# Performance work log

Measured on AMD Instinct MI355X. Metric: run time of the kernel, lower is better.

Reference implementation:

```python
import jax, jax.numpy as jnp
import numpy as np

PHI = (1.0 + 5.0 ** 0.5) / 2.0
B, S, V, D, N, L = 8, 128, 32000, 256, 256, 2


def silu(x):
    return x * jax.nn.sigmoid(x)


def setup_inputs() -> dict:
    key = jax.random.key(0)
    ks = jax.random.split(key, 9)
    inp = {}
    inp["input_ids"] = jax.random.randint(ks[0], (B, S), 0, V)
    # token embedding, init std=0.02 as in _init_weights
    inp["emb"] = 0.02 * jax.random.normal(ks[1], (V, 2 * D), jnp.float32)
    # per-layer resonant params, stacked over layer dim L
    inp["ip_w"] = 0.02 * jax.random.normal(ks[2], (L, D, 2 * D), jnp.float32)  # input_proj weight
    inp["ip_b"] = jnp.zeros((L, D), jnp.float32)                                # input_proj bias
    inp["Wn"] = 0.02 * jax.random.normal(ks[3], (L, N, D), jnp.float32)         # W parameter
    inp["Bn"] = jnp.zeros((L, N, D), jnp.float32)                               # B parameter
    inp["opr"] = 0.02 * jax.random.normal(ks[4], (L, D, N), jnp.float32)        # out_proj_real
    inp["opi"] = 0.02 * jax.random.normal(ks[5], (L, D, N), jnp.float32)        # out_proj_imag
    inp["out_w"] = 0.02 * jax.random.normal(ks[6], (V, 2 * D), jnp.float32)     # output_proj
    inp["out_b"] = jnp.zeros((V,), jnp.float32)
    return inp


def _forward(input_ids, emb, ip_w, ip_b, Wn, Bn, opr, opi, out_w, out_b):
    tok = emb[input_ids]                                  # [B, S, 2D]
    w_emb = jnp.transpose(tok[..., :D], (1, 0, 2))        # [S, B, D] (time-major for scan)
    b_emb = jnp.transpose(tok[..., D:], (1, 0, 2))        # [S, B, D]
    ts = jnp.arange(S, dtype=jnp.float32)                 # t values

    def step(carry, xs):
        h_r, h_i = carry
        w_t, b_t, t = xs
        t_phi = t * PHI
        # Euler transform of recurrent state
        wl = 1.0 + jnp.abs(w_t)                           # [B, D]
        th_r = h_r / wl + b_t + t_phi
        th_i = h_i / wl + b_t + t_phi
        sr, cr = jnp.sin(th_r), jnp.cos(th_r)
        si, ci = jnp.sin(th_i), jnp.cos(th_i)
        h_r_new = cr * ci - sr * si                       # complex rotate
        h_i_new = cr * si + sr * ci
        x_r, x_i = h_r_new, h_i_new
        # resonant layers (residual deltas)
        for l in range(L):
            xc = jnp.concatenate([x_r, x_i], axis=-1) @ ip_w[l].T + ip_b[l]   # [B, D]
            wl_n = 1.0 + jnp.abs(Wn[l])                                        # [N, D]
            theta = xc[:, None, :] / wl_n + Bn[l] + t_phi                      # [B, N, D]
            cos_sum = jnp.cos(theta).sum(-1)                                   # [B, N]
            sin_sum = jnp.sin(theta).sum(-1)                                   # [B, N]
            x_r = x_r + silu(cos_sum @ opr[l].T)
            x_i = x_i + silu(sin_sum @ opi[l].T)
        logits = jnp.concatenate([x_r, x_i], axis=-1) @ out_w.T + out_b       # [B, V]
        return (h_r_new, h_i_new), logits

    h0 = jnp.zeros((B, D), jnp.float32)
    (_, _), logits = jax.lax.scan(step, (h0, h0), (w_emb, b_emb, ts))
    return jnp.transpose(logits, (1, 0, 2))               # [B, S, V]


def reference(input_ids, emb, ip_w, ip_b, Wn, Bn, opr, opi, out_w, out_b):
    return _forward(input_ids, emb, ip_w, ip_b, Wn, Bn, opr, opi, out_w, out_b)
```

## Files before the change

### kernel.cpp

```cpp
#include <hip/hip_runtime.h>
#include <hip/hip_fp16.h>
#include <math.h>


#define PHIF 1.6180339887498949f

typedef unsigned short u16;
typedef __attribute__((ext_vector_type(8))) _Float16 f16x8;
typedef __attribute__((ext_vector_type(4))) float f32x4;

constexpr int B = 8, S = 128, V = 32000, D = 256, N = 256, L = 2;
constexpr int TWO_D = 512;
constexpr int M = S * B;

constexpr size_t OFF_XR   = 0;
constexpr size_t OFF_XI   = OFF_XR   + (size_t)M * D;
constexpr size_t OFF_XC   = OFF_XI   + (size_t)M * D;
constexpr size_t OFF_CS   = OFF_XC   + (size_t)M * D;
constexpr size_t OFF_SS   = OFF_CS   + (size_t)M * N;
constexpr size_t OFF_RWT  = OFF_SS   + (size_t)M * N;
constexpr size_t OFF_BNT  = OFF_RWT  + (size_t)L * N * D;
constexpr size_t OFF_IPWT = OFF_BNT  + (size_t)L * N * D;
constexpr size_t OFF_OPRT = OFF_IPWT + (size_t)L * TWO_D * D;
constexpr size_t OFF_OPIT = OFF_OPRT + (size_t)L * N * D;
constexpr size_t OFF_FLT_END = OFF_OPIT + (size_t)L * N * D;

constexpr size_t A2_BYTE_OFF = OFF_FLT_END * 4;
constexpr size_t W2_BYTE_OFF = A2_BYTE_OFF + (size_t)M * 512 * 2;
constexpr size_t WS_NEED     = W2_BYTE_OFF + (size_t)V * 512 * 2;

__device__ __forceinline__ u16 f2h(float x) {
    return __half_as_ushort(__float2half(x));
}

__global__ __launch_bounds__(256) void prepconv_kernel(const float* __restrict__ Wn,
                                                       const float* __restrict__ Bn,
                                                       const float* __restrict__ ip_w,
                                                       const float* __restrict__ opr,
                                                       const float* __restrict__ opi,
                                                       const float* __restrict__ out_w,
                                                       float* __restrict__ ws,
                                                       u16* __restrict__ W2) {
    int blk = blockIdx.x;
    if (blk < 1024) {
        int i = blk * 256 + threadIdx.x;
        if (i < L * N * D) {
            int l = i >> 16;
            int r = i & 65535;
            int a = r >> 8;
            int c = r & 255;
            float wv = Wn[(size_t)l * N * D + (size_t)c * D + a];
            ws[OFF_RWT + i] = 1.0f / (1.0f + fabsf(wv));
            ws[OFF_BNT + i] = Bn[(size_t)l * N * D + (size_t)c * D + a];
            ws[OFF_OPRT + i] = opr[(size_t)l * D * N + (size_t)c * N + a];
            ws[OFF_OPIT + i] = opi[(size_t)l * D * N + (size_t)c * N + a];
        }
        int l = i >> 17;
        int r = i & 131071;
        int k = r >> 8;
        int d = r & 255;
        ws[OFF_IPWT + i] = ip_w[(size_t)l * D * TWO_D + (size_t)d * TWO_D + k];
    } else {
        int gid = (blk - 1024) * 256 + threadIdx.x;
        if (gid >= V * 128) return;
        int v  = gid >> 7;
        int kq = (gid & 127) << 2;
        float4 x = *(const float4*)&out_w[(size_t)v * TWO_D + kq];
        ushort4 h = {f2h(x.x), f2h(x.y), f2h(x.z), f2h(x.w)};
        *(ushort4*)&W2[(size_t)v * 512 + kq] = h;
    }
}

__global__ __launch_bounds__(64) void recur_kernel(const int* __restrict__ ids,
                                                   const float* __restrict__ emb,
                                                   float* __restrict__ ws) {
    __shared__ int   sid[S];
    __shared__ float swv[S][64];
    __shared__ float sbv[S][64];
    int lane = threadIdx.x;
    int blk  = blockIdx.x;
    int b  = blk >> 2;
    int d  = (blk & 3) * 64 + lane;
    sid[lane]      = ids[b * S + lane];
    sid[64 + lane] = ids[b * S + 64 + lane];
    __syncthreads();
    #pragma unroll 16
    for (int t = 0; t < S; ++t) {
        const float* e = emb + (size_t)sid[t] * TWO_D;
        swv[t][lane] = e[d];
        sbv[t][lane] = e[D + d];
    }
    __syncthreads();
    float* XR = ws + OFF_XR;
    float* XI = ws + OFF_XI;
    float u = 0.f;
    #pragma unroll 8
    for (int t = 0; t < S; ++t) {
        float wl = 1.0f + fabsf(swv[t][lane]);
        float c  = 2.0f * sbv[t][lane] + (2.0f * PHIF) * (float)t;
        float psi = __fdividef(u, wl) + c;
        float sn = __sinf(psi);
        float cs = __cosf(psi);
        size_t row = (size_t)(t * B + b) * D + d;
        XR[row] = cs;
        XI[row] = sn;
        u = cs + sn;
    }
}

__global__ __launch_bounds__(256) void layers_kernel(const float* __restrict__ ipb,
                                                     float* __restrict__ ws,
                                                     u16* __restrict__ A2,
                                                     int use_a2) {
    __shared__ float xr[4][D];
    __shared__ float xi[4][D];
    __shared__ float xc[4][D];
    __shared__ float cs[4][N];
    __shared__ float ss[4][N];
    int m0 = blockIdx.x * 4;
    int tid = threadIdx.x;

    #pragma unroll
    for (int r = 0; r < 4; ++r) {
        xr[r][tid] = ws[OFF_XR + (size_t)(m0 + r) * D + tid];
        xi[r][tid] = ws[OFF_XI + (size_t)(m0 + r) * D + tid];
    }
    float tp[4];
    #pragma unroll
    for (int r = 0; r < 4; ++r) tp[r] = (float)((m0 + r) >> 3) * PHIF;

    for (int l = 0; l < L; ++l) {
        __syncthreads();
        const float* WT = ws + OFF_IPWT + (size_t)l * TWO_D * D;
        float bias = ipb[l * D + tid];
        float a[4];
        #pragma unroll
        for (int r = 0; r < 4; ++r) a[r] = bias;
        #pragma unroll 4
        for (int k = 0; k < D; ++k) {
            float wv = WT[k * D + tid];
            #pragma unroll
            for (int r = 0; r < 4; ++r) a[r] = fmaf(xr[r][k], wv, a[r]);
        }
        #pragma unroll 4
        for (int k = 0; k < D; ++k) {
            float wv = WT[(k + D) * D + tid];
            #pragma unroll
            for (int r = 0; r < 4; ++r) a[r] = fmaf(xi[r][k], wv, a[r]);
        }
        #pragma unroll
        for (int r = 0; r < 4; ++r) xc[r][tid] = a[r];
        __syncthreads();

        const float* RW = ws + OFF_RWT + (size_t)l * D * N;
        const float* BN = ws + OFF_BNT + (size_t)l * D * N;
        float ac[4] = {0.f, 0.f, 0.f, 0.f};
        float as[4] = {0.f, 0.f, 0.f, 0.f};
        #pragma unroll 2
        for (int d = 0; d < D; ++d) {
            float rw = RW[d * N + tid];
            float bn = BN[d * N + tid];
            #pragma unroll
            for (int r = 0; r < 4; ++r) {
                float th = fmaf(xc[r][d], rw, bn) + tp[r];
                ac[r] += __cosf(th);
                as[r] += __sinf(th);
            }
        }
        #pragma unroll
        for (int r = 0; r < 4; ++r) { cs[r][tid] = ac[r]; ss[r][tid] = as[r]; }
        __syncthreads();

        const float* WR = ws + OFF_OPRT + (size_t)l * N * D;
        const float* WI = ws + OFF_OPIT + (size_t)l * N * D;
        float ur[4] = {0.f, 0.f, 0.f, 0.f};
        float ui[4] = {0.f, 0.f, 0.f, 0.f};
        #pragma unroll 4
        for (int n = 0; n < N; ++n) {
            float wr = WR[n * D + tid];
            float wi = WI[n * D + tid];
            #pragma unroll
            for (int r = 0; r < 4; ++r) {
                ur[r] = fmaf(cs[r][n], wr, ur[r]);
                ui[r] = fmaf(ss[r][n], wi, ui[r]);
            }
        }
        #pragma unroll
        for (int r = 0; r < 4; ++r) {
            float vr = ur[r], vi = ui[r];
            float sgr = 1.0f / (1.0f + expf(-vr));
            float sgi = 1.0f / (1.0f + expf(-vi));
            xr[r][tid] += vr * sgr;
            xi[r][tid] += vi * sgi;
        }
    }
    __syncthreads();
    #pragma unroll
    for (int r = 0; r < 4; ++r) {
        ws[OFF_XR + (size_t)(m0 + r) * D + tid] = xr[r][tid];
        ws[OFF_XI + (size_t)(m0 + r) * D + tid] = xi[r][tid];
    }
    if (use_a2) {
        #pragma unroll
        for (int r = 0; r < 4; ++r) {
            A2[(size_t)(m0 + r) * 512 + tid]       = f2h(xr[r][tid]);
            A2[(size_t)(m0 + r) * 512 + 256 + tid] = f2h(xi[r][tid]);
        }
    }
}

__global__ __launch_bounds__(256) void logits_mfma_kernel(const u16* __restrict__ A2,
                                                          const u16* __restrict__ W2,
                                                          const float* __restrict__ out_b,
                                                          float* __restrict__ out) {
    __shared__ u16 sA[128 * 32];
    __shared__ u16 sW[128 * 32];
    int rb = blockIdx.x & 7;
    int cb = blockIdx.x >> 3;
    int tid = threadIdx.x;
    int w = tid >> 6, l = tid & 63;
    int wr = w >> 1, wc = w & 1;

    f32x4 acc[4][4];
    #pragma unroll
    for (int i = 0; i < 4; ++i)
        #pragma unroll
        for (int j = 0; j < 4; ++j) acc[i][j] = (f32x4){0.f, 0.f, 0.f, 0.f};

    int srow = l >> 2;
    int sko  = (l & 3) * 8;
    int kg = (l >> 4) * 8;
    int rl = l & 15;

    for (int kk = 0; kk < 512; kk += 32) {
        #pragma unroll
        for (int j = 0; j < 2; ++j) {
            int rloc = (w * 2 + j) * 16 + srow;
            const u16* sa = A2 + (size_t)(rb * 128 + rloc) * 512 + kk + sko;
            const u16* sw = W2 + (size_t)(cb * 128 + rloc) * 512 + kk + sko;
            u16* da = &sA[rloc * 32 + sko];
            u16* dw = &sW[rloc * 32 + sko];
            __builtin_amdgcn_global_load_lds((const __attribute__((address_space(1))) void*)sa,
                                             (__attribute__((address_space(3))) void*)da, 16, 0, 0);
            __builtin_amdgcn_global_load_lds((const __attribute__((address_space(1))) void*)sw,
                                             (__attribute__((address_space(3))) void*)dw, 16, 0, 0);
        }
        __syncthreads();
        f16x8 af[4], wf[4];
        #pragma unroll
        for (int f = 0; f < 4; ++f) {
            af[f] = *(const f16x8*)&sA[(wr * 64 + f * 16 + rl) * 32 + kg];
            wf[f] = *(const f16x8*)&sW[(wc * 64 + f * 16 + rl) * 32 + kg];
        }
        #pragma unroll
        for (int fr = 0; fr < 4; ++fr)
            #pragma unroll
            for (int fc = 0; fc < 4; ++fc)
                acc[fr][fc] = __builtin_amdgcn_mfma_f32_16x16x32_f16(
                    af[fr], wf[fc], acc[fr][fc], 0, 0, 0);
        __syncthreads();
    }

    int rq = l >> 4;
    #pragma unroll
    for (int fc = 0; fc < 4; ++fc) {
        int v = cb * 128 + wc * 64 + fc * 16 + rl;
        float bv = out_b[v];
        #pragma unroll
        for (int fr = 0; fr < 4; ++fr) {
            #pragma unroll
            for (int r = 0; r < 4; ++r) {
                int row = rb * 128 + wr * 64 + fr * 16 + rq * 4 + r;
                int t = row >> 3, b = row & 7;
                out[((size_t)(b * S + t)) * V + v] = acc[fr][fc][r] + bv;
            }
        }
    }
}

constexpr int GBM = 256, GBN = 64, GBK = 32;
constexpr int LDA = GBM + 4;
constexpr int LDW = GBN + 4;

__global__ __launch_bounds__(256) void logits_kernel(const float* __restrict__ out_w,
                                                     const float* __restrict__ out_b,
                                                     const float* __restrict__ ws,
                                                     float* __restrict__ out) {
    __shared__ float As[GBK][LDA];
    __shared__ float Wsh[GBK][LDW];
    const float* XR = ws + OFF_XR;
    const float* XI = ws + OFF_XI;
    int cb = blockIdx.x % (V / GBN);
    int rb = blockIdx.x / (V / GBN);
    int tid = threadIdx.x;
    int tx = tid & 7;
    int ty = tid >> 3;
    int m_base = ty * 8;
    int n0 = tx * 8;
    float acc[8][8];
    #pragma unroll
    for (int r = 0; r < 8; ++r)
        #pragma unroll
        for (int c = 0; c < 8; ++c) acc[r][c] = 0.f;

    for (int kc = 0; kc < TWO_D; kc += GBK) {
        #pragma unroll
        for (int j = 0; j < 32; ++j) {
            int idx = tid + j * 256;
            int k = idx & 31;
            int m = idx >> 5;
            int kgl = kc + k;
            int row = rb * GBM + m;
            As[k][m] = (kgl < D) ? XR[row * D + kgl] : XI[row * D + (kgl - D)];
        }
        #pragma unroll
        for (int j = 0; j < 8; ++j) {
            int idx = tid + j * 256;
            int k = idx & 31;
            int n = idx >> 5;
            Wsh[k][n] = out_w[(size_t)(cb * GBN + n) * TWO_D + kc + k];
        }
        __syncthreads();
        #pragma unroll 8
        for (int k = 0; k < GBK; ++k) {
            float4 a0 = *(const float4*)&As[k][m_base];
            float4 a1 = *(const float4*)&As[k][m_base + 4];
            float4 w0 = *(const float4*)&Wsh[k][n0];
            float4 w1 = *(const float4*)&Wsh[k][n0 + 4];
            float am[8] = {a0.x, a0.y, a0.z, a0.w, a1.x, a1.y, a1.z, a1.w};
            float wn[8] = {w0.x, w0.y, w0.z, w0.w, w1.x, w1.y, w1.z, w1.w};
            #pragma unroll
            for (int r = 0; r < 8; ++r)
                #pragma unroll
                for (int c = 0; c < 8; ++c)
                    acc[r][c] = fmaf(am[r], wn[c], acc[r][c]);
        }
        __syncthreads();
    }
    int v0 = cb * GBN + n0;
    float4 ob0 = *(const float4*)&out_b[v0];
    float4 ob1 = *(const float4*)&out_b[v0 + 4];
    float obn[8] = {ob0.x, ob0.y, ob0.z, ob0.w, ob1.x, ob1.y, ob1.z, ob1.w};
    #pragma unroll
    for (int r = 0; r < 8; ++r) {
        int row = rb * GBM + m_base + r;
        int t = row >> 3;
        int b = row & 7;
        float o[8];
        #pragma unroll
        for (int c = 0; c < 8; ++c) o[c] = acc[r][c] + obn[c];
        *(float4*)&out[((size_t)(b * S + t)) * V + v0]     = *(float4*)&o[0];
        *(float4*)&out[((size_t)(b * S + t)) * V + v0 + 4] = *(float4*)&o[4];
    }
}

extern "C" void kernel_launch(void* const* d_in, const int* in_sizes, int n_in,
                              void* d_out, int out_size, void* d_ws, size_t ws_size,
                              hipStream_t stream) {
    const int*   ids   = (const int*)d_in[0];
    const float* emb   = (const float*)d_in[1];
    const float* ip_w  = (const float*)d_in[2];
    const float* ip_b  = (const float*)d_in[3];
    const float* Wn    = (const float*)d_in[4];
    const float* Bn    = (const float*)d_in[5];
    const float* opr   = (const float*)d_in[6];
    const float* opi   = (const float*)d_in[7];
    const float* out_w = (const float*)d_in[8];
    const float* out_b = (const float*)d_in[9];
    float* out = (float*)d_out;
    float* ws  = (float*)d_ws;
    const bool use_mfma = (ws_size >= WS_NEED);
    u16* A2 = (u16*)((char*)d_ws + A2_BYTE_OFF);
    u16* W2 = (u16*)((char*)d_ws + W2_BYTE_OFF);

    int prep_blocks = 1024 + (use_mfma ? (V * 128 / 256) : 0);
    hipLaunchKernelGGL(prepconv_kernel, dim3(prep_blocks), dim3(256), 0, stream,
                       Wn, Bn, ip_w, opr, opi, out_w, ws, W2);
    hipLaunchKernelGGL(recur_kernel, dim3(32), dim3(64), 0, stream, ids, emb, ws);
    hipLaunchKernelGGL(layers_kernel, dim3(M / 4), dim3(256), 0, stream,
                       ip_b, ws, A2, use_mfma ? 1 : 0);
    if (use_mfma) {
        hipLaunchKernelGGL(logits_mfma_kernel, dim3((V / 128) * (M / 128)), dim3(256), 0, stream,
                           A2, W2, out_b, out);
    } else {
        hipLaunchKernelGGL(logits_kernel, dim3((V / GBN) * (M / GBM)), dim3(256), 0, stream,
                           out_w, out_b, ws, out);
    }
}
```

Baseline: 521.4 us.

## Split layers_kernel reductions across two thread halves with shared-memory partial sums

```diff
diff --git a/kernel.cpp b/kernel.cpp
--- a/kernel.cpp
+++ b/kernel.cpp
@@ -108,7 +108,7 @@
     }
 }
 
-__global__ __launch_bounds__(256) void layers_kernel(const float* __restrict__ ipb,
+__global__ __launch_bounds__(512) void layers_kernel(const float* __restrict__ ipb,
                                                      float* __restrict__ ws,
                                                      u16* __restrict__ A2,
                                                      int use_a2) {
@@ -117,13 +117,17 @@
     __shared__ float xc[4][D];
     __shared__ float cs[4][N];
     __shared__ float ss[4][N];
+    __shared__ float p0[4][N];
+    __shared__ float p1[4][N];
     int m0 = blockIdx.x * 4;
     int tid = threadIdx.x;
-
-    #pragma unroll
-    for (int r = 0; r < 4; ++r) {
-        xr[r][tid] = ws[OFF_XR + (size_t)(m0 + r) * D + tid];
-        xi[r][tid] = ws[OFF_XI + (size_t)(m0 + r) * D + tid];
+    int half = tid >> 8;
+    int id = tid & 255;
+
+    for (int e = tid; e < 4 * D; e += 512) {
+        int r = e >> 8, d = e & 255;
+        xr[r][d] = ws[OFF_XR + (size_t)(m0 + r) * D + d];
+        xi[r][d] = ws[OFF_XI + (size_t)(m0 + r) * D + d];
     }
     float tp[4];
     #pragma unroll
@@ -132,79 +136,114 @@
     for (int l = 0; l < L; ++l) {
         __syncthreads();
         const float* WT = ws + OFF_IPWT + (size_t)l * TWO_D * D;
-        float bias = ipb[l * D + tid];
-        float a[4];
-        #pragma unroll
-        for (int r = 0; r < 4; ++r) a[r] = bias;
-        #pragma unroll 4
-        for (int k = 0; k < D; ++k) {
-            float wv = WT[k * D + tid];
-            #pragma unroll
-            for (int r = 0; r < 4; ++r) a[r] = fmaf(xr[r][k], wv, a[r]);
-        }
-        #pragma unroll 4
-        for (int k = 0; k < D; ++k) {
-            float wv = WT[(k + D) * D + tid];
-            #pragma unroll
-            for (int r = 0; r < 4; ++r) a[r] = fmaf(xi[r][k], wv, a[r]);
-        }
-        #pragma unroll
-        for (int r = 0; r < 4; ++r) xc[r][tid] = a[r];
+        {
+            float a[4] = {0.f, 0.f, 0.f, 0.f};
+            if (half == 0) {
+                #pragma unroll 8
+                for (int k = 0; k < D; ++k) {
+                    float wv = WT[k * D + id];
+                    #pragma unroll
+                    for (int r = 0; r < 4; ++r) a[r] = fmaf(xr[r][k], wv, a[r]);
+                }
+                #pragma unroll
+                for (int r = 0; r < 4; ++r) xc[r][id] = a[r];
+            } else {
+                #pragma unroll 8
+                for (int k = 0; k < D; ++k) {
+                    float wv = WT[(k + D) * D + id];
+                    #pragma unroll
+                    for (int r = 0; r < 4; ++r) a[r] = fmaf(xi[r][k], wv, a[r]);
+                }
+                #pragma unroll
+                for (int r = 0; r < 4; ++r) p0[r][id] = a[r];
+            }
+        }
+        __syncthreads();
+        for (int e = tid; e < 4 * D; e += 512) {
+            int r = e >> 8, d = e & 255;
+            xc[r][d] += p0[r][d] + ipb[l * D + d];
+        }
         __syncthreads();
 
         const float* RW = ws + OFF_RWT + (size_t)l * D * N;
         const float* BN = ws + OFF_BNT + (size_t)l * D * N;
-        float ac[4] = {0.f, 0.f, 0.f, 0.f};
-        float as[4] = {0.f, 0.f, 0.f, 0.f};
-        #pragma unroll 2
-        for (int d = 0; d < D; ++d) {
-            float rw = RW[d * N + tid];
-            float bn = BN[d * N + tid];
-            #pragma unroll
-            for (int r = 0; r < 4; ++r) {
-                float th = fmaf(xc[r][d], rw, bn) + tp[r];
-                ac[r] += __cosf(th);
-                as[r] += __sinf(th);
-            }
-        }
-        #pragma unroll
-        for (int r = 0; r < 4; ++r) { cs[r][tid] = ac[r]; ss[r][tid] = as[r]; }
+        {
+            float ac[4] = {0.f, 0.f, 0.f, 0.f};
+            float av[4] = {0.f, 0.f, 0.f, 0.f};
+            int dbase = half * 128;
+            #pragma unroll 8
+            for (int dd = 0; dd < 128; ++dd) {
+                int d = dbase + dd;
+                float rw = RW[d * N + id];
+                float bn = BN[d * N + id];
+                #pragma unroll
+                for (int r = 0; r < 4; ++r) {
+                    float th = fmaf(xc[r][d], rw, bn) + tp[r];
+                    ac[r] += __cosf(th);
+                    av[r] += __sinf(th);
+                }
+            }
+            if (half == 0) {
+                #pragma unroll
+                for (int r = 0; r < 4; ++r) { cs[r][id] = ac[r]; ss[r][id] = av[r]; }
+            } else {
+                #pragma unroll
+                for (int r = 0; r < 4; ++r) { p0[r][id] = ac[r]; p1[r][id] = av[r]; }
+            }
+        }
+        __syncthreads();
+        for (int e = tid; e < 4 * N; e += 512) {
+            int r = e >> 8, n = e & 255;
+            cs[r][n] += p0[r][n];
+            ss[r][n] += p1[r][n];
+        }
         __syncthreads();
 
         const float* WR = ws + OFF_OPRT + (size_t)l * N * D;
         const float* WI = ws + OFF_OPIT + (size_t)l * N * D;
-        float ur[4] = {0.f, 0.f, 0.f, 0.f};
-        float ui[4] = {0.f, 0.f, 0.f, 0.f};
-        #pragma unroll 4
-        for (int n = 0; n < N; ++n) {
-            float wr = WR[n * D + tid];
-            float wi = WI[n * D + tid];
-            #pragma unroll
-            for (int r = 0; r < 4; ++r) {
-                ur[r] = fmaf(cs[r][n], wr, ur[r]);
-                ui[r] = fmaf(ss[r][n], wi, ui[r]);
-            }
-        }
-        #pragma unroll
-        for (int r = 0; r < 4; ++r) {
-            float vr = ur[r], vi = ui[r];
-            float sgr = 1.0f / (1.0f + expf(-vr));
-            float sgi = 1.0f / (1.0f + expf(-vi));
-            xr[r][tid] += vr * sgr;
-            xi[r][tid] += vi * sgi;
+        {
+            float ur[4] = {0.f, 0.f, 0.f, 0.f};
+            float ui[4] = {0.f, 0.f, 0.f, 0.f};
+            int nbase = half * 128;
+            #pragma unroll 8
+            for (int nn = 0; nn < 128; ++nn) {
+                int n = nbase + nn;
+                float wr = WR[n * D + id];
+                float wi = WI[n * D + id];
+                #pragma unroll
+                for (int r = 0; r < 4; ++r) {
+                    ur[r] = fmaf(cs[r][n], wr, ur[r]);
+                    ui[r] = fmaf(ss[r][n], wi, ui[r]);
+                }
+            }
+            if (half == 1) {
+                #pragma unroll
+                for (int r = 0; r < 4; ++r) { p0[r][id] = ur[r]; p1[r][id] = ui[r]; }
+            }
+            __syncthreads();
+            if (half == 0) {
+                #pragma unroll
+                for (int r = 0; r < 4; ++r) {
+                    float vr = ur[r] + p0[r][id];
+                    float vi = ui[r] + p1[r][id];
+                    float sgr = 1.0f / (1.0f + expf(-vr));
+                    float sgi = 1.0f / (1.0f + expf(-vi));
+                    xr[r][id] += vr * sgr;
+                    xi[r][id] += vi * sgi;
+                }
+            }
         }
     }
     __syncthreads();
-    #pragma unroll
-    for (int r = 0; r < 4; ++r) {
-        ws[OFF_XR + (size_t)(m0 + r) * D + tid] = xr[r][tid];
-        ws[OFF_XI + (size_t)(m0 + r) * D + tid] = xi[r][tid];
-    }
-    if (use_a2) {
-        #pragma unroll
-        for (int r = 0; r < 4; ++r) {
-            A2[(size_t)(m0 + r) * 512 + tid]       = f2h(xr[r][tid]);
-            A2[(size_t)(m0 + r) * 512 + 256 + tid] = f2h(xi[r][tid]);
+    for (int e = tid; e < 4 * D; e += 512) {
+        int r = e >> 8, d = e & 255;
+        float vr = xr[r][d];
+        float vi = xi[r][d];
+        ws[OFF_XR + (size_t)(m0 + r) * D + d] = vr;
+        ws[OFF_XI + (size_t)(m0 + r) * D + d] = vi;
+        if (use_a2) {
+            A2[(size_t)(m0 + r) * 512 + d]       = f2h(vr);
+            A2[(size_t)(m0 + r) * 512 + 256 + d] = f2h(vi);
         }
     }
 }
@@ -377,7 +416,7 @@
     hipLaunchKernelGGL(prepconv_kernel, dim3(prep_blocks), dim3(256), 0, stream,
                        Wn, Bn, ip_w, opr, opi, out_w, ws, W2);
     hipLaunchKernelGGL(recur_kernel, dim3(32), dim3(64), 0, stream, ids, emb, ws);
-    hipLaunchKernelGGL(layers_kernel, dim3(M / 4), dim3(256), 0, stream,
+    hipLaunchKernelGGL(layers_kernel, dim3(M / 4), dim3(512), 0, stream,
                        ip_b, ws, A2, use_mfma ? 1 : 0);
     if (use_mfma) {
         hipLaunchKernelGGL(logits_mfma_kernel, dim3((V / 128) * (M / 128)), dim3(256), 0, stream,
```

Result: faster. 481.6 us (-7.6%).
